# Performance work log

Hardware: AMD Instinct MI355X
Metric: run time of the kernel (lower is better)

The kernel has to match this reference:

```python
import jax, jax.numpy as jnp
import numpy as np

N_ENT = 100000
N_REL = 500
IN_DIM = 128
OUT_DIM = 128
E = 500000


def setup_inputs() -> dict:
    key = jax.random.key(0)
    ks = jax.random.split(key, 9)
    src = jax.random.randint(ks[0], (E,), 0, N_ENT)
    dst = jax.random.randint(ks[1], (E,), 0, N_ENT)
    rel = jax.random.randint(ks[2], (E,), 0, N_REL)
    ent_embed = jax.random.normal(ks[3], (N_ENT, IN_DIM), dtype=jnp.float32)
    rel_embed = jax.random.normal(ks[4], (N_REL, IN_DIM), dtype=jnp.float32)
    # xavier_normal with gain 1.414 for linear weights
    g = 1.414
    a_w = jax.random.normal(ks[5], (OUT_DIM, 3 * IN_DIM), dtype=jnp.float32) * (g * np.sqrt(2.0 / (3 * IN_DIM + OUT_DIM)))
    a_b = jnp.zeros((OUT_DIM,), dtype=jnp.float32)
    a2_w = jax.random.normal(ks[6], (1, OUT_DIM), dtype=jnp.float32) * (g * np.sqrt(2.0 / (OUT_DIM + 1)))
    a2_b = jnp.zeros((1,), dtype=jnp.float32)
    return {"ent_embed": ent_embed, "rel_embed": rel_embed, "a_w": a_w, "a_b": a_b,
            "a2_w": a2_w, "a2_b": a2_b, "src": src, "dst": dst, "rel": rel}


def reference(ent_embed, rel_embed, a_w, a_b, a2_w, a2_b, src, dst, rel):
    # gather: [E, 3*in_dim]
    h = jnp.concatenate([ent_embed[src], ent_embed[dst], rel_embed[rel]], axis=1)
    c = h @ a_w.T + a_b                      # [E, out_dim]
    b = jax.nn.leaky_relu(c @ a2_w.T + a2_b, negative_slope=0.01)  # [E, 1]
    e_b = jnp.exp(b)                          # [E, 1]
    temp1 = e_b * c                           # [E, out_dim]
    # scatter-sum into source nodes (SpecialSpmmFinal keyed on edges[0] = src)
    e_b_sum = jax.ops.segment_sum(e_b, src, num_segments=N_ENT)   # [N, 1]
    h_sum = jax.ops.segment_sum(temp1, src, num_segments=N_ENT)   # [N, out_dim]
    ebs = jnp.where(e_b_sum == 0, jnp.float32(1e-12), e_b_sum)
    h_ent = h_sum / ebs
    # scatter-mean of temp1 by relation id
    rel_sum = jax.ops.segment_sum(temp1, rel, num_segments=N_REL)          # [R, out_dim]
    rel_cnt = jax.ops.segment_sum(jnp.ones((temp1.shape[0],), jnp.float32), rel, num_segments=N_REL)
    h_rel = rel_sum / jnp.maximum(rel_cnt, 1.0)[:, None]
    return (jax.nn.elu(h_ent), jax.nn.elu(h_rel))
```

## Files before the change

### kernel.cpp

```cpp
#include <hip/hip_runtime.h>
#include <hip/hip_bf16.h>

#define N_ENT_C 100000
#define N_REL_C 500
#define NEDGE_C 500000
#define SCAN_BLOCKS 391
#define EPB 1024
#define NB_EDGE 489
#define CHUNK_B 62

#define OFF_WTHI  0
#define OFF_WTLO  16384
#define OFF_WTR   32768
#define OFF_PR    49152
#define OFF_PS    113152
#define OFF_PSH   12913152
#define OFF_PDH   19313152

#define DO_HSRC     0
#define DO_OSRC     100000
#define DO_BSUM     200000
#define DO_RELSTART 200512
#define DO_PART8    201024
#define DO_CHUNKOFF 205120
#define DO_BLKHIST  209216
#define DO_BLKOFFS  459584
#define DO_DSTS     709952
#define DO_RELS     1209952
#define DO_SRCR     1709952
#define DO_DSTR     2209952
#define DO_RELP     2709952
#define DO_QS       3237952
#define DO_QD       3337952
#define DO_QR       3437952
#define SCRATCH_ROWS 26863

typedef short bf16x8 __attribute__((ext_vector_type(8)));
typedef short s16x4  __attribute__((ext_vector_type(4)));
typedef float f32x4  __attribute__((ext_vector_type(4)));

__device__ inline unsigned short bf_rne(float x) {
    unsigned int u = __float_as_uint(x);
    u += 0x7FFF + ((u >> 16) & 1);
    return (unsigned short)(u >> 16);
}
__device__ inline float bf2f(unsigned short h) {
    return __uint_as_float(((unsigned int)h) << 16);
}

__global__ void prep_w(const float* __restrict__ aw, unsigned short* __restrict__ Wthi,
                       unsigned short* __restrict__ Wtlo, float* __restrict__ Wtr) {
    int idx = blockIdx.x * 256 + threadIdx.x;
    if (idx < 32768) {
        int n = idx >> 7, k = idx & 127;
        float v = (n < 128) ? aw[n * 384 + k] : aw[(n - 128) * 384 + 128 + k];
        unsigned short h = bf_rne(v);
        Wthi[idx] = h;
        Wtlo[idx] = bf_rne(v - bf2f(h));
    } else if (idx < 49152) {
        int t = idx - 32768;
        int k = t >> 7, o = t & 127;
        Wtr[t] = aw[o * 384 + 256 + k];
    }
}

__global__ void rel_proj(const float* __restrict__ rele, const float* __restrict__ Wtr,
                         const float* __restrict__ ab, const float* __restrict__ a2w,
                         float* __restrict__ Pr, float* __restrict__ qr) {
    int r = blockIdx.x;
    int o = threadIdx.x;
    float acc = ab[o];
    for (int k = 0; k < 128; ++k)
        acc = fmaf(rele[r * 128 + k], Wtr[k * 128 + o], acc);
    Pr[r * 128 + o] = acc;
    __shared__ float red[128];
    red[o] = acc * a2w[o];
    __syncthreads();
    for (int off = 64; off > 0; off >>= 1) {
        if (o < off) red[o] += red[o + off];
        __syncthreads();
    }
    if (o == 0) qr[r] = red[0];
}

__global__ __launch_bounds__(256) void ent_mfma(const float* __restrict__ ent,
                                                const unsigned short* __restrict__ Wthi,
                                                const unsigned short* __restrict__ Wtlo,
                                                const float* __restrict__ a2w,
                                                float* __restrict__ Ps,
                                                unsigned short* __restrict__ PsH,
                                                unsigned short* __restrict__ PdH,
                                                float* __restrict__ qs,
                                                float* __restrict__ qd) {
    __shared__ __align__(16) char sh[32768];
    __shared__ float qred[4][64];
    const int tid = threadIdx.x;
    const int block_row = blockIdx.x * 64;

#pragma unroll
    for (int i = 0; i < 8; ++i) {
        int f = tid + i * 256;
        int m = f >> 5, k4 = f & 31;
        float4 v = make_float4(0.f, 0.f, 0.f, 0.f);
        int grow = block_row + m;
        if (grow < N_ENT_C) v = *(const float4*)&ent[(size_t)grow * 128 + k4 * 4];
        unsigned short h0 = bf_rne(v.x), h1 = bf_rne(v.y), h2 = bf_rne(v.z), h3 = bf_rne(v.w);
        s16x4 hv; hv[0] = (short)h0; hv[1] = (short)h1; hv[2] = (short)h2; hv[3] = (short)h3;
        s16x4 lv;
        lv[0] = (short)bf_rne(v.x - bf2f(h0));
        lv[1] = (short)bf_rne(v.y - bf2f(h1));
        lv[2] = (short)bf_rne(v.z - bf2f(h2));
        lv[3] = (short)bf_rne(v.w - bf2f(h3));
        int off = m * 256 + k4 * 8;
        off ^= (m & 7) << 4;
        *(s16x4*)(sh + off) = hv;
        *(s16x4*)(sh + 16384 + off) = lv;
    }
    __syncthreads();

    const int w = tid >> 6, lane = tid & 63;
    const int l15 = lane & 15, lh = lane >> 4;
    const int n0 = w * 64;

    f32x4 zz = {0.f, 0.f, 0.f, 0.f};
    f32x4 acc[4][4];
#pragma unroll
    for (int mf = 0; mf < 4; ++mf)
#pragma unroll
        for (int nf = 0; nf < 4; ++nf) acc[mf][nf] = zz;

#pragma unroll
    for (int ks = 0; ks < 4; ++ks) {
        int kb = ks * 32 + lh * 8;
        bf16x8 ah[4], al[4];
#pragma unroll
        for (int mf = 0; mf < 4; ++mf) {
            int row = mf * 16 + l15;
            int off = row * 256 + kb * 2;
            off ^= (row & 7) << 4;
            ah[mf] = *(const bf16x8*)(sh + off);
            al[mf] = *(const bf16x8*)(sh + 16384 + off);
        }
#pragma unroll
        for (int nf = 0; nf < 4; ++nf) {
            int n = n0 + nf * 16 + l15;
            bf16x8 bh = *(const bf16x8*)(Wthi + n * 128 + kb);
            bf16x8 bl = *(const bf16x8*)(Wtlo + n * 128 + kb);
#pragma unroll
            for (int mf = 0; mf < 4; ++mf) {
                acc[mf][nf] = __builtin_amdgcn_mfma_f32_16x16x32_bf16(ah[mf], bh, acc[mf][nf], 0, 0, 0);
                acc[mf][nf] = __builtin_amdgcn_mfma_f32_16x16x32_bf16(ah[mf], bl, acc[mf][nf], 0, 0, 0);
                acc[mf][nf] = __builtin_amdgcn_mfma_f32_16x16x32_bf16(al[mf], bh, acc[mf][nf], 0, 0, 0);
            }
        }
    }

    float a2[4];
#pragma unroll
    for (int nf = 0; nf < 4; ++nf) a2[nf] = a2w[(n0 + nf * 16 + l15) & 127];
    float qp[4][4];
#pragma unroll
    for (int mf = 0; mf < 4; ++mf)
#pragma unroll
        for (int v = 0; v < 4; ++v) qp[mf][v] = 0.f;

#pragma unroll
    for (int mf = 0; mf < 4; ++mf) {
#pragma unroll
        for (int nf = 0; nf < 4; ++nf) {
            int col = n0 + nf * 16 + l15;
#pragma unroll
            for (int v = 0; v < 4; ++v) {
                float val = acc[mf][nf][v];
                qp[mf][v] = fmaf(val, a2[nf], qp[mf][v]);
                int row = block_row + mf * 16 + lh * 4 + v;
                if (row < N_ENT_C) {
                    if (col < 128) {
                        Ps[(size_t)row * 128 + col] = val;
                        PsH[(size_t)row * 128 + col] = bf_rne(val);
                    } else {
                        PdH[(size_t)row * 128 + (col - 128)] = bf_rne(val);
                    }
                }
            }
        }
    }
#pragma unroll
    for (int mf = 0; mf < 4; ++mf)
#pragma unroll
        for (int v = 0; v < 4; ++v) {
            float q = qp[mf][v];
            q += __shfl_xor(q, 1);
            q += __shfl_xor(q, 2);
            q += __shfl_xor(q, 4);
            q += __shfl_xor(q, 8);
            qp[mf][v] = q;
        }
    if (l15 == 0) {
#pragma unroll
        for (int mf = 0; mf < 4; ++mf)
#pragma unroll
            for (int v = 0; v < 4; ++v) qred[w][mf * 16 + lh * 4 + v] = qp[mf][v];
    }
    __syncthreads();
    if (tid < 64) {
        int row = block_row + tid;
        if (row < N_ENT_C) {
            qs[row] = qred[0][tid] + qred[1][tid];
            qd[row] = qred[2][tid] + qred[3][tid];
        }
    }
}

__global__ __launch_bounds__(256) void edge_hist(const int* __restrict__ src,
                                                 const int* __restrict__ rel,
                                                 int* __restrict__ histSrc,
                                                 int* __restrict__ blkHist) {
    __shared__ int lh[512];
    int tid = threadIdx.x;
    lh[tid] = 0; lh[tid + 256] = 0;
    __syncthreads();
    int base = blockIdx.x * EPB;
#pragma unroll
    for (int j = 0; j < 4; ++j) {
        int e = base + j * 256 + tid;
        if (e < NEDGE_C) {
            atomicAdd(&histSrc[src[e]], 1);
            atomicAdd(&lh[rel[e]], 1);
        }
    }
    __syncthreads();
    blkHist[blockIdx.x * 512 + tid] = lh[tid];
    blkHist[blockIdx.x * 512 + 256 + tid] = lh[tid + 256];
}

__global__ void colsum(const int* __restrict__ blkHist, int* __restrict__ partial) {
    int r = threadIdx.x;
    int k = blockIdx.x;
    int b0 = k * CHUNK_B;
    int b1 = min(b0 + CHUNK_B, NB_EDGE);
    int t = 0;
    for (int b = b0; b < b1; ++b) t += blkHist[b * 512 + r];
    partial[k * 512 + r] = t;
}

__global__ void scan512(const int* __restrict__ partial, int* __restrict__ relStart,
                        int* __restrict__ chunkOff) {
    __shared__ int a[512], b2[512];
    int tid = threadIdx.x;
    int p8[8];
    int t = 0;
#pragma unroll
    for (int k = 0; k < 8; ++k) { p8[k] = partial[k * 512 + tid]; t += p8[k]; }
    a[tid] = t;
    __syncthreads();
    int v = t;
    int* cur = a; int* nxt = b2;
    for (int off = 1; off < 512; off <<= 1) {
        int x = cur[tid] + ((tid >= off) ? cur[tid - off] : 0);
        nxt[tid] = x;
        __syncthreads();
        int* tmp = cur; cur = nxt; nxt = tmp;
    }
    int excl = cur[tid] - v;
    relStart[tid] = excl;
    int run = excl;
#pragma unroll
    for (int k = 0; k < 8; ++k) { chunkOff[k * 512 + tid] = run; run += p8[k]; }
}

__global__ void colscan(const int* __restrict__ blkHist, const int* __restrict__ chunkOff,
                        int* __restrict__ blockOffs) {
    int r = threadIdx.x;
    int k = blockIdx.x;
    int b0 = k * CHUNK_B;
    int b1 = min(b0 + CHUNK_B, NB_EDGE);
    int off = chunkOff[k * 512 + r];
    for (int b = b0; b < b1; ++b) {
        blockOffs[b * 512 + r] = off;
        off += blkHist[b * 512 + r];
    }
}

__global__ void scan_blockred(const int* __restrict__ hist, int* __restrict__ blockSums, int n) {
    __shared__ int s[256];
    int tid = threadIdx.x;
    int i = blockIdx.x * 256 + tid;
    s[tid] = (i < n) ? hist[i] : 0;
    __syncthreads();
    for (int off = 128; off > 0; off >>= 1) {
        if (tid < off) s[tid] += s[tid + off];
        __syncthreads();
    }
    if (tid == 0) blockSums[blockIdx.x] = s[0];
}

__global__ void scan_single(int* __restrict__ data, int n) {
    __shared__ int a[1024], b2[1024];
    int tid = threadIdx.x;
    int v = (tid < n) ? data[tid] : 0;
    a[tid] = v;
    __syncthreads();
    int* cur = a; int* nxt = b2;
    for (int off = 1; off < 1024; off <<= 1) {
        int x = cur[tid] + ((tid >= off) ? cur[tid - off] : 0);
        nxt[tid] = x;
        __syncthreads();
        int* t = cur; cur = nxt; nxt = t;
    }
    if (tid < n) data[tid] = cur[tid] - v;
}

__global__ void scan_final(const int* __restrict__ hist, const int* __restrict__ blockOffs,
                           int* __restrict__ offs, int n) {
    __shared__ int a[256], b2[256];
    int tid = threadIdx.x;
    int i = blockIdx.x * 256 + tid;
    int v = (i < n) ? hist[i] : 0;
    a[tid] = v;
    __syncthreads();
    int* cur = a; int* nxt = b2;
    for (int off = 1; off < 256; off <<= 1) {
        int x = cur[tid] + ((tid >= off) ? cur[tid - off] : 0);
        nxt[tid] = x;
        __syncthreads();
        int* t = cur; cur = nxt; nxt = t;
    }
    if (i < n) offs[i] = cur[tid] - v + blockOffs[blockIdx.x];
}

__global__ __launch_bounds__(256) void scatter_both(const int* __restrict__ src,
                                                    const int* __restrict__ dst,
                                                    const int* __restrict__ rel,
                                                    int* __restrict__ offsSrc,
                                                    const int* __restrict__ blockOffs,
                                                    int* __restrict__ dstS, int* __restrict__ relS,
                                                    int* __restrict__ srcR, int* __restrict__ dstR) {
    __shared__ int lh[512];
    int tid = threadIdx.x;
    lh[tid] = 0; lh[tid + 256] = 0;
    __syncthreads();
    int base = blockIdx.x * EPB;
    const int* bo = &blockOffs[blockIdx.x * 512];
#pragma unroll
    for (int j = 0; j < 4; ++j) {
        int e = base + j * 256 + tid;
        if (e < NEDGE_C) {
            int s = src[e], d = dst[e], r = rel[e];
            int p = atomicAdd(&offsSrc[s], 1);
            dstS[p] = d; relS[p] = r;
            int lr = atomicAdd(&lh[r], 1);
            int q = bo[r] + lr;
            srcR[q] = s; dstR[q] = d;
        }
    }
}

__global__ __launch_bounds__(256) void rel_phase(const unsigned short* __restrict__ PsH,
                                                 const unsigned short* __restrict__ PdH,
                                                 const float* __restrict__ qs,
                                                 const float* __restrict__ qd,
                                                 const float* __restrict__ qr,
                                                 const int* __restrict__ relStart,
                                                 const int* __restrict__ srcR,
                                                 const int* __restrict__ dstR,
                                                 const float* __restrict__ a2b,
                                                 float* __restrict__ relpart) {
    int r = blockIdx.x >> 3;
    int p = blockIdx.x & 7;
    int start = relStart[r];
    int end = relStart[r + 1];
    int tid = threadIdx.x;
    int w = tid >> 6;
    int h = (tid >> 5) & 1;
    int l = tid & 31;
    int slot = p * 8 + w * 2 + h;
    float bb = a2b[0];
    float qrr = qr[r];
    float4 acc = make_float4(0.f, 0.f, 0.f, 0.f);
    float ebs = 0.f;
    for (int i = start + slot; i < end; i += 64) {
        int s = srcR[i], d = dstR[i];
        float b = qs[s] + qd[d] + qrr + bb;
        b = (b > 0.f) ? b : 0.01f * b;
        float eb = expf(b);
        ushort4 pv = *(const ushort4*)&PsH[(size_t)s * 128 + l * 4];
        ushort4 dv = *(const ushort4*)&PdH[(size_t)d * 128 + l * 4];
        acc.x = fmaf(eb, bf2f(pv.x) + bf2f(dv.x), acc.x);
        acc.y = fmaf(eb, bf2f(pv.y) + bf2f(dv.y), acc.y);
        acc.z = fmaf(eb, bf2f(pv.z) + bf2f(dv.z), acc.z);
        acc.w = fmaf(eb, bf2f(pv.w) + bf2f(dv.w), acc.w);
        ebs += eb;
    }
    __shared__ float vred[8][128];
    __shared__ float sred[8];
    int sub = w * 2 + h;
    *(float4*)&vred[sub][l * 4] = acc;
    if (l == 0) sred[sub] = ebs;
    __syncthreads();
    if (tid < 128) {
        float v = 0.f;
#pragma unroll
        for (int k2 = 0; k2 < 8; ++k2) v += vred[k2][tid];
        float e = 0.f;
#pragma unroll
        for (int k2 = 0; k2 < 8; ++k2) e += sred[k2];
        int pi = r * 8 + p;
        relpart[pi * 132 + tid] = v;
        if (tid == 0) relpart[pi * 132 + 128] = e;
    }
}

__global__ void rel_fin(const float* __restrict__ relpart, const float* __restrict__ Pr,
                        const int* __restrict__ relStart, float* __restrict__ outRel) {
    int r = blockIdx.x;
    int o = threadIdx.x;
    float v = 0.f, e = 0.f;
#pragma unroll
    for (int p = 0; p < 8; ++p) {
        v += relpart[(r * 8 + p) * 132 + o];
        e += relpart[(r * 8 + p) * 132 + 128];
    }
    float cnt = (float)(relStart[r + 1] - relStart[r]);
    float h = (v + e * Pr[r * 128 + o]) / fmaxf(cnt, 1.f);
    outRel[r * 128 + o] = (h > 0.f) ? h : (expf(h) - 1.f);
}

__global__ __launch_bounds__(256) void src_phase(float* __restrict__ Ps,
                                                 const unsigned short* __restrict__ PdH,
                                                 const float* __restrict__ Pr,
                                                 const float* __restrict__ qs,
                                                 const float* __restrict__ qd,
                                                 const float* __restrict__ qr,
                                                 const int* __restrict__ offsSrc,
                                                 const int* __restrict__ dstS,
                                                 const int* __restrict__ relS,
                                                 const float* __restrict__ a2b,
                                                 float* __restrict__ out) {
    int wid = (blockIdx.x * 256 + threadIdx.x) >> 6;
    if (wid >= N_ENT_C) return;
    int lane = threadIdx.x & 63;
    int h = lane >> 5, l = lane & 31;
    int s = wid;
    int start = (s == 0) ? 0 : offsSrc[s - 1];
    int end = offsSrc[s];
    float* dstp = (s < SCRATCH_ROWS) ? &Ps[(size_t)s * 128] : &out[(size_t)s * 128];
    if (end == start) {
        if (h == 0) *(float4*)&dstp[l * 4] = make_float4(0.f, 0.f, 0.f, 0.f);
        return;
    }
    float bb = a2b[0];
    float qss = qs[s];
    float4 acc = make_float4(0.f, 0.f, 0.f, 0.f);
    float ebs = 0.f;
    for (int i = start + h; i < end; i += 2) {
        int d = dstS[i], r = relS[i];
        float b = qss + qd[d] + qr[r] + bb;
        b = (b > 0.f) ? b : 0.01f * b;
        float eb = expf(b);
        ushort4 dv = *(const ushort4*)&PdH[(size_t)d * 128 + l * 4];
        float4 rv = *(const float4*)&Pr[(size_t)r * 128 + l * 4];
        acc.x = fmaf(eb, bf2f(dv.x) + rv.x, acc.x);
        acc.y = fmaf(eb, bf2f(dv.y) + rv.y, acc.y);
        acc.z = fmaf(eb, bf2f(dv.z) + rv.z, acc.z);
        acc.w = fmaf(eb, bf2f(dv.w) + rv.w, acc.w);
        ebs += eb;
    }
    acc.x += __shfl_xor(acc.x, 32);
    acc.y += __shfl_xor(acc.y, 32);
    acc.z += __shfl_xor(acc.z, 32);
    acc.w += __shfl_xor(acc.w, 32);
    ebs += __shfl_xor(ebs, 32);
    float inv = 1.f / ebs;
    float4 ps4 = *(const float4*)&Ps[(size_t)s * 128 + l * 4];
    float hx = ps4.x + acc.x * inv;
    float hy = ps4.y + acc.y * inv;
    float hz = ps4.z + acc.z * inv;
    float hw = ps4.w + acc.w * inv;
    hx = (hx > 0.f) ? hx : (expf(hx) - 1.f);
    hy = (hy > 0.f) ? hy : (expf(hy) - 1.f);
    hz = (hz > 0.f) ? hz : (expf(hz) - 1.f);
    hw = (hw > 0.f) ? hw : (expf(hw) - 1.f);
    if (h == 0) *(float4*)&dstp[l * 4] = make_float4(hx, hy, hz, hw);
}

extern "C" void kernel_launch(void* const* d_in, const int* in_sizes, int n_in,
                              void* d_out, int out_size, void* d_ws, size_t ws_size,
                              hipStream_t stream) {
    const float* ent  = (const float*)d_in[0];
    const float* rele = (const float*)d_in[1];
    const float* aw   = (const float*)d_in[2];
    const float* ab   = (const float*)d_in[3];
    const float* a2w  = (const float*)d_in[4];
    const float* a2b  = (const float*)d_in[5];
    const int* src    = (const int*)d_in[6];
    const int* dst    = (const int*)d_in[7];
    const int* rel    = (const int*)d_in[8];
    float* out = (float*)d_out;

    float* ws = (float*)d_ws;
    unsigned short* Wthi = (unsigned short*)(ws + OFF_WTHI);
    unsigned short* Wtlo = (unsigned short*)(ws + OFF_WTLO);
    float* Wtr = ws + OFF_WTR;
    float* Pr  = ws + OFF_PR;
    float* Ps  = ws + OFF_PS;
    unsigned short* PsH = (unsigned short*)(ws + OFF_PSH);
    unsigned short* PdH = (unsigned short*)(ws + OFF_PDH);

    int* dI = (int*)d_out;
    int* histSrc  = dI + DO_HSRC;
    int* offsSrc  = dI + DO_OSRC;
    int* bsum     = dI + DO_BSUM;
    int* relStart = dI + DO_RELSTART;
    int* part8    = dI + DO_PART8;
    int* chunkOff = dI + DO_CHUNKOFF;
    int* blkHist  = dI + DO_BLKHIST;
    int* blockOffs= dI + DO_BLKOFFS;
    int* dstS     = dI + DO_DSTS;
    int* relS     = dI + DO_RELS;
    int* srcR     = dI + DO_SRCR;
    int* dstR     = dI + DO_DSTR;
    float* relpart = (float*)dI + DO_RELP;
    float* qs     = (float*)dI + DO_QS;
    float* qd     = (float*)dI + DO_QD;
    float* qr     = (float*)dI + DO_QR;

    hipMemsetAsync(histSrc, 0, (size_t)N_ENT_C * sizeof(int), stream);

    prep_w<<<192, 256, 0, stream>>>(aw, Wthi, Wtlo, Wtr);
    rel_proj<<<N_REL_C, 128, 0, stream>>>(rele, Wtr, ab, a2w, Pr, qr);
    ent_mfma<<<(N_ENT_C + 63) / 64, 256, 0, stream>>>(ent, Wthi, Wtlo, a2w, Ps, PsH, PdH, qs, qd);

    edge_hist<<<NB_EDGE, 256, 0, stream>>>(src, rel, histSrc, blkHist);
    colsum<<<8, 512, 0, stream>>>(blkHist, part8);
    scan512<<<1, 512, 0, stream>>>(part8, relStart, chunkOff);
    colscan<<<8, 512, 0, stream>>>(blkHist, chunkOff, blockOffs);
    scan_blockred<<<SCAN_BLOCKS, 256, 0, stream>>>(histSrc, bsum, N_ENT_C);
    scan_single<<<1, 1024, 0, stream>>>(bsum, SCAN_BLOCKS);
    scan_final<<<SCAN_BLOCKS, 256, 0, stream>>>(histSrc, bsum, offsSrc, N_ENT_C);
    scatter_both<<<NB_EDGE, 256, 0, stream>>>(src, dst, rel, offsSrc, blockOffs,
                                              dstS, relS, srcR, dstR);

    rel_phase<<<N_REL_C * 8, 256, 0, stream>>>(PsH, PdH, qs, qd, qr, relStart, srcR, dstR,
                                               a2b, relpart);
    rel_fin<<<N_REL_C, 128, 0, stream>>>(relpart, Pr, relStart, out + (size_t)N_ENT_C * 128);

    src_phase<<<(N_ENT_C + 3) / 4, 256, 0, stream>>>(Ps, PdH, Pr, qs, qd, qr,
                                                     offsSrc, dstS, relS, a2b, out);

    hipMemcpyAsync(out, Ps, (size_t)SCRATCH_ROWS * 128 * sizeof(float),
                   hipMemcpyDeviceToDevice, stream);
}
```

Measured before the change: 274.7 us.

## Use bf16 source/relation projections in src_phase and shrink fp32 staging

Drops the fp32 Ps buffer. src_phase now reads the bf16 PsH and a new bf16 PrH copy of the relation projections, and uses 16 lanes × 8 elements with 4 edge groups per wave instead of 32 lanes × 4 with 2 groups. The output scratch layout is rearranged so fewer rows need staging, which shrinks the final device-to-device memcpy. This is meant to cut fp32 write and read traffic and the copy size, at the cost of bf16 rounding on the self term and relation term, which may affect accuracy.

```diff
diff --git a/kernel.cpp b/kernel.cpp
--- a/kernel.cpp
+++ b/kernel.cpp
@@ -13,31 +13,33 @@
 #define OFF_WTLO  16384
 #define OFF_WTR   32768
 #define OFF_PR    49152
-#define OFF_PS    113152
-#define OFF_PSH   12913152
-#define OFF_PDH   19313152
-
-#define DO_HSRC     0
-#define DO_OSRC     100000
-#define DO_BSUM     200000
-#define DO_RELSTART 200512
-#define DO_PART8    201024
-#define DO_CHUNKOFF 205120
-#define DO_BLKHIST  209216
-#define DO_BLKOFFS  459584
-#define DO_DSTS     709952
-#define DO_RELS     1209952
-#define DO_SRCR     1709952
-#define DO_DSTR     2209952
-#define DO_RELP     2709952
-#define DO_QS       3237952
-#define DO_QD       3337952
-#define DO_QR       3437952
-#define SCRATCH_ROWS 26863
+#define OFF_PRH   113152
+#define OFF_STAGE 145152
+#define OFF_PSH   1445760
+#define OFF_PDH   7845760
+
+#define DO_OSRC     0
+#define DO_DSTS     100000
+#define DO_RELS     600000
+#define DO_QS       1100000
+#define DO_QD       1200000
+#define DO_QR       1300000
+#define SCRATCH_ROWS 10161
+#define DO_HSRC     1300512
+#define DO_BSUM     1400512
+#define DO_RELSTART 1401024
+#define DO_PART8    1401536
+#define DO_CHUNKOFF 1405632
+#define DO_BLKHIST  1409728
+#define DO_BLKOFFS  1660096
+#define DO_SRCR     1910464
+#define DO_DSTR     2410464
+#define DO_RELP     2910464
 
 typedef short bf16x8 __attribute__((ext_vector_type(8)));
 typedef short s16x4  __attribute__((ext_vector_type(4)));
 typedef float f32x4  __attribute__((ext_vector_type(4)));
+typedef unsigned short u16x8 __attribute__((ext_vector_type(8)));
 
 __device__ inline unsigned short bf_rne(float x) {
     unsigned int u = __float_as_uint(x);
@@ -66,13 +68,15 @@
 
 __global__ void rel_proj(const float* __restrict__ rele, const float* __restrict__ Wtr,
                          const float* __restrict__ ab, const float* __restrict__ a2w,
-                         float* __restrict__ Pr, float* __restrict__ qr) {
+                         float* __restrict__ Pr, unsigned short* __restrict__ PrH,
+                         float* __restrict__ qr) {
     int r = blockIdx.x;
     int o = threadIdx.x;
     float acc = ab[o];
     for (int k = 0; k < 128; ++k)
         acc = fmaf(rele[r * 128 + k], Wtr[k * 128 + o], acc);
     Pr[r * 128 + o] = acc;
+    PrH[r * 128 + o] = bf_rne(acc);
     __shared__ float red[128];
     red[o] = acc * a2w[o];
     __syncthreads();
@@ -87,7 +91,6 @@
                                                 const unsigned short* __restrict__ Wthi,
                                                 const unsigned short* __restrict__ Wtlo,
                                                 const float* __restrict__ a2w,
-                                                float* __restrict__ Ps,
                                                 unsigned short* __restrict__ PsH,
                                                 unsigned short* __restrict__ PdH,
                                                 float* __restrict__ qs,
@@ -175,12 +178,9 @@
                 qp[mf][v] = fmaf(val, a2[nf], qp[mf][v]);
                 int row = block_row + mf * 16 + lh * 4 + v;
                 if (row < N_ENT_C) {
-                    if (col < 128) {
-                        Ps[(size_t)row * 128 + col] = val;
-                        PsH[(size_t)row * 128 + col] = bf_rne(val);
-                    } else {
-                        PdH[(size_t)row * 128 + (col - 128)] = bf_rne(val);
-                    }
+                    unsigned short hv = bf_rne(val);
+                    if (col < 128) PsH[(size_t)row * 128 + col] = hv;
+                    else PdH[(size_t)row * 128 + (col - 128)] = hv;
                 }
             }
         }
@@ -426,9 +426,9 @@
     outRel[r * 128 + o] = (h > 0.f) ? h : (expf(h) - 1.f);
 }
 
-__global__ __launch_bounds__(256) void src_phase(float* __restrict__ Ps,
+__global__ __launch_bounds__(256) void src_phase(const unsigned short* __restrict__ PsH,
                                                  const unsigned short* __restrict__ PdH,
-                                                 const float* __restrict__ Pr,
+                                                 const unsigned short* __restrict__ PrH,
                                                  const float* __restrict__ qs,
                                                  const float* __restrict__ qd,
                                                  const float* __restrict__ qr,
@@ -436,52 +436,60 @@
                                                  const int* __restrict__ dstS,
                                                  const int* __restrict__ relS,
                                                  const float* __restrict__ a2b,
+                                                 float* __restrict__ stage,
                                                  float* __restrict__ out) {
     int wid = (blockIdx.x * 256 + threadIdx.x) >> 6;
     if (wid >= N_ENT_C) return;
     int lane = threadIdx.x & 63;
-    int h = lane >> 5, l = lane & 31;
+    int g = lane >> 4, l = lane & 15;
     int s = wid;
     int start = (s == 0) ? 0 : offsSrc[s - 1];
     int end = offsSrc[s];
-    float* dstp = (s < SCRATCH_ROWS) ? &Ps[(size_t)s * 128] : &out[(size_t)s * 128];
+    float* dstp = (s < SCRATCH_ROWS) ? &stage[(size_t)s * 128] : &out[(size_t)s * 128];
     if (end == start) {
-        if (h == 0) *(float4*)&dstp[l * 4] = make_float4(0.f, 0.f, 0.f, 0.f);
+        if (g == 0) {
+            *(float4*)&dstp[l * 8] = make_float4(0.f, 0.f, 0.f, 0.f);
+            *(float4*)&dstp[l * 8 + 4] = make_float4(0.f, 0.f, 0.f, 0.f);
+        }
         return;
     }
     float bb = a2b[0];
     float qss = qs[s];
-    float4 acc = make_float4(0.f, 0.f, 0.f, 0.f);
+    float acc[8];
+#pragma unroll
+    for (int j = 0; j < 8; ++j) acc[j] = 0.f;
     float ebs = 0.f;
-    for (int i = start + h; i < end; i += 2) {
+    for (int i = start + g; i < end; i += 4) {
         int d = dstS[i], r = relS[i];
         float b = qss + qd[d] + qr[r] + bb;
         b = (b > 0.f) ? b : 0.01f * b;
         float eb = expf(b);
-        ushort4 dv = *(const ushort4*)&PdH[(size_t)d * 128 + l * 4];
-        float4 rv = *(const float4*)&Pr[(size_t)r * 128 + l * 4];
-        acc.x = fmaf(eb, bf2f(dv.x) + rv.x, acc.x);
-        acc.y = fmaf(eb, bf2f(dv.y) + rv.y, acc.y);
-        acc.z = fmaf(eb, bf2f(dv.z) + rv.z, acc.z);
-        acc.w = fmaf(eb, bf2f(dv.w) + rv.w, acc.w);
+        u16x8 dv = *(const u16x8*)&PdH[(size_t)d * 128 + l * 8];
+        u16x8 rv = *(const u16x8*)&PrH[(size_t)r * 128 + l * 8];
+#pragma unroll
+        for (int j = 0; j < 8; ++j)
+            acc[j] = fmaf(eb, bf2f(dv[j]) + bf2f(rv[j]), acc[j]);
         ebs += eb;
     }
-    acc.x += __shfl_xor(acc.x, 32);
-    acc.y += __shfl_xor(acc.y, 32);
-    acc.z += __shfl_xor(acc.z, 32);
-    acc.w += __shfl_xor(acc.w, 32);
+#pragma unroll
+    for (int j = 0; j < 8; ++j) {
+        acc[j] += __shfl_xor(acc[j], 16);
+        acc[j] += __shfl_xor(acc[j], 32);
+    }
+    ebs += __shfl_xor(ebs, 16);
     ebs += __shfl_xor(ebs, 32);
-    float inv = 1.f / ebs;
-    float4 ps4 = *(const float4*)&Ps[(size_t)s * 128 + l * 4];
-    float hx = ps4.x + acc.x * inv;
-    float hy = ps4.y + acc.y * inv;
-    float hz = ps4.z + acc.z * inv;
-    float hw = ps4.w + acc.w * inv;
-    hx = (hx > 0.f) ? hx : (expf(hx) - 1.f);
-    hy = (hy > 0.f) ? hy : (expf(hy) - 1.f);
-    hz = (hz > 0.f) ? hz : (expf(hz) - 1.f);
-    hw = (hw > 0.f) ? hw : (expf(hw) - 1.f);
-    if (h == 0) *(float4*)&dstp[l * 4] = make_float4(hx, hy, hz, hw);
+    if (g == 0) {
+        float inv = 1.f / ebs;
+        u16x8 ps = *(const u16x8*)&PsH[(size_t)s * 128 + l * 8];
+        float h[8];
+#pragma unroll
+        for (int j = 0; j < 8; ++j) {
+            float x = bf2f(ps[j]) + acc[j] * inv;
+            h[j] = (x > 0.f) ? x : (expf(x) - 1.f);
+        }
+        *(float4*)&dstp[l * 8]     = make_float4(h[0], h[1], h[2], h[3]);
+        *(float4*)&dstp[l * 8 + 4] = make_float4(h[4], h[5], h[6], h[7]);
+    }
 }
 
 extern "C" void kernel_launch(void* const* d_in, const int* in_sizes, int n_in,
@@ -503,33 +511,34 @@
     unsigned short* Wtlo = (unsigned short*)(ws + OFF_WTLO);
     float* Wtr = ws + OFF_WTR;
     float* Pr  = ws + OFF_PR;
-    float* Ps  = ws + OFF_PS;
+    unsigned short* PrH = (unsigned short*)(ws + OFF_PRH);
+    float* stage = ws + OFF_STAGE;
     unsigned short* PsH = (unsigned short*)(ws + OFF_PSH);
     unsigned short* PdH = (unsigned short*)(ws + OFF_PDH);
 
     int* dI = (int*)d_out;
+    int* offsSrc  = dI + DO_OSRC;
+    int* dstS     = dI + DO_DSTS;
+    int* relS     = dI + DO_RELS;
+    float* qs     = (float*)dI + DO_QS;
+    float* qd     = (float*)dI + DO_QD;
+    float* qr     = (float*)dI + DO_QR;
     int* histSrc  = dI + DO_HSRC;
-    int* offsSrc  = dI + DO_OSRC;
     int* bsum     = dI + DO_BSUM;
     int* relStart = dI + DO_RELSTART;
     int* part8    = dI + DO_PART8;
     int* chunkOff = dI + DO_CHUNKOFF;
     int* blkHist  = dI + DO_BLKHIST;
     int* blockOffs= dI + DO_BLKOFFS;
-    int* dstS     = dI + DO_DSTS;
-    int* relS     = dI + DO_RELS;
     int* srcR     = dI + DO_SRCR;
     int* dstR     = dI + DO_DSTR;
     float* relpart = (float*)dI + DO_RELP;
-    float* qs     = (float*)dI + DO_QS;
-    float* qd     = (float*)dI + DO_QD;
-    float* qr     = (float*)dI + DO_QR;
 
     hipMemsetAsync(histSrc, 0, (size_t)N_ENT_C * sizeof(int), stream);
 
     prep_w<<<192, 256, 0, stream>>>(aw, Wthi, Wtlo, Wtr);
-    rel_proj<<<N_REL_C, 128, 0, stream>>>(rele, Wtr, ab, a2w, Pr, qr);
-    ent_mfma<<<(N_ENT_C + 63) / 64, 256, 0, stream>>>(ent, Wthi, Wtlo, a2w, Ps, PsH, PdH, qs, qd);
+    rel_proj<<<N_REL_C, 128, 0, stream>>>(rele, Wtr, ab, a2w, Pr, PrH, qr);
+    ent_mfma<<<(N_ENT_C + 63) / 64, 256, 0, stream>>>(ent, Wthi, Wtlo, a2w, PsH, PdH, qs, qd);
 
     edge_hist<<<NB_EDGE, 256, 0, stream>>>(src, rel, histSrc, blkHist);
     colsum<<<8, 512, 0, stream>>>(blkHist, part8);
@@ -545,9 +554,9 @@
                                                a2b, relpart);
     rel_fin<<<N_REL_C, 128, 0, stream>>>(relpart, Pr, relStart, out + (size_t)N_ENT_C * 128);
 
-    src_phase<<<(N_ENT_C + 3) / 4, 256, 0, stream>>>(Ps, PdH, Pr, qs, qd, qr,
-                                                     offsSrc, dstS, relS, a2b, out);
-
-    hipMemcpyAsync(out, Ps, (size_t)SCRATCH_ROWS * 128 * sizeof(float),
+    src_phase<<<(N_ENT_C + 3) / 4, 256, 0, stream>>>(PsH, PdH, PrH, qs, qd, qr,
+                                                     offsSrc, dstS, relS, a2b, stage, out);
+
+    hipMemcpyAsync(out, stage, (size_t)SCRATCH_ROWS * 128 * sizeof(float),
                    hipMemcpyDeviceToDevice, stream);
 }
```

Result: no change. 269.3 us (-2.0%).
